# Kernel optimization log

Measured on AMD Instinct MI355X. Metric: run time of the kernel, lower is better.

Reference implementation:

```python
import jax, jax.numpy as jnp
import numpy as np

N_NODES = 100000
N_EDGES = 625000
D_IN = 128
D_OUT = 128


def setup_inputs() -> dict:
    key = jax.random.key(0)
    k1, k2, k3, k4, k5 = jax.random.split(key, 5)
    scale = 1.0 / np.sqrt(D_IN)
    x = jax.random.normal(k1, (N_NODES, D_IN), dtype=jnp.float32)
    edge_index = jax.random.randint(k2, (2, N_EDGES), 0, N_NODES, dtype=jnp.int64)
    W_l = jax.random.normal(k3, (D_IN, D_OUT), dtype=jnp.float32) * scale
    b_l = jax.random.normal(k4, (D_OUT,), dtype=jnp.float32) * scale
    W_r = jax.random.normal(k5, (D_IN, D_OUT), dtype=jnp.float32) * scale
    return {"x": x, "edge_index": edge_index, "W_l": W_l, "b_l": b_l, "W_r": W_r}


def reference(x, edge_index, W_l, b_l, W_r):
    # SAGEConv (mean aggr, no self loops):
    #   out = lin_l(mean_{j in N(i)} x_j) + lin_r(x_i)
    src = edge_index[0]  # message source nodes
    dst = edge_index[1]  # aggregation targets
    n = x.shape[0]
    msgs = x[src]  # [E, D_IN] gather
    agg = jax.ops.segment_sum(msgs, dst, num_segments=n)  # [N, D_IN]
    deg = jax.ops.segment_sum(jnp.ones_like(dst, dtype=x.dtype), dst, num_segments=n)
    mean = agg / jnp.maximum(deg, 1.0)[:, None]  # isolated nodes -> 0
    return mean @ W_l + b_l + x @ W_r
```

## Files before the change

### kernel.cpp

```cpp
#include <hip/hip_runtime.h>


constexpr int N_NODES = 100000;
constexpr int N_EDGES = 625000;
constexpr int D = 128;
constexpr int SCAN_CHUNK = 1024;
constexpr int N_SCAN_BLOCKS = (N_NODES + SCAN_CHUNK - 1) / SCAN_CHUNK;

typedef __attribute__((ext_vector_type(8))) short short8;
typedef __attribute__((ext_vector_type(4))) short short4v;
typedef __attribute__((ext_vector_type(4))) float f32x4;

__device__ __forceinline__ unsigned short f2bf(float f) {
    union { float f; unsigned int u; } c; c.f = f;
    unsigned int u = c.u + 0x7fffu + ((c.u >> 16) & 1u);
    return (unsigned short)(u >> 16);
}

__global__ __launch_bounds__(256) void csr_hist(
    const int* __restrict__ dst, int* __restrict__ cnt)
{
    int e = blockIdx.x * 256 + threadIdx.x;
    if (e < N_EDGES) atomicAdd(&cnt[dst[e]], 1);
}

__global__ __launch_bounds__(256) void scan_blocks(
    const int* __restrict__ cnt, int* __restrict__ ptr, int* __restrict__ bsums)
{
    __shared__ int sh[256];
    const int t = threadIdx.x;
    const int base = blockIdx.x * SCAN_CHUNK + t * 4;
    int v0 = (base + 0 < N_NODES) ? cnt[base + 0] : 0;
    int v1 = (base + 1 < N_NODES) ? cnt[base + 1] : 0;
    int v2 = (base + 2 < N_NODES) ? cnt[base + 2] : 0;
    int v3 = (base + 3 < N_NODES) ? cnt[base + 3] : 0;
    const int tsum = v0 + v1 + v2 + v3;
    sh[t] = tsum;
    __syncthreads();
    #pragma unroll
    for (int off = 1; off < 256; off <<= 1) {
        int val = (t >= off) ? sh[t - off] : 0;
        __syncthreads();
        sh[t] += val;
        __syncthreads();
    }
    const int texcl = sh[t] - tsum;
    if (t == 255) bsums[blockIdx.x] = sh[255];
    int e0 = texcl, e1 = e0 + v0, e2 = e1 + v1, e3 = e2 + v2;
    if (base + 0 < N_NODES) ptr[base + 0] = e0;
    if (base + 1 < N_NODES) ptr[base + 1] = e1;
    if (base + 2 < N_NODES) ptr[base + 2] = e2;
    if (base + 3 < N_NODES) ptr[base + 3] = e3;
}

__global__ __launch_bounds__(128) void scan_bsums(int* __restrict__ bsums)
{
    __shared__ int sh[128];
    const int t = threadIdx.x;
    int v = (t < N_SCAN_BLOCKS) ? bsums[t] : 0;
    sh[t] = v;
    __syncthreads();
    #pragma unroll
    for (int off = 1; off < 128; off <<= 1) {
        int val = (t >= off) ? sh[t - off] : 0;
        __syncthreads();
        sh[t] += val;
        __syncthreads();
    }
    if (t < N_SCAN_BLOCKS) bsums[t] = sh[t] - v;
}

__global__ __launch_bounds__(256) void add_offsets(
    int* __restrict__ ptr, int* __restrict__ cursor, const int* __restrict__ bsums)
{
    int i = blockIdx.x * 256 + threadIdx.x;
    if (i < N_NODES) {
        int p = ptr[i] + bsums[i >> 10];
        ptr[i] = p;
        cursor[i] = p;
    }
    if (i == 0) ptr[N_NODES] = N_EDGES;
}

__global__ __launch_bounds__(256) void csr_fill(
    const int* __restrict__ src, const int* __restrict__ dst,
    int* __restrict__ cursor, int* __restrict__ sorted_src)
{
    int e = blockIdx.x * 256 + threadIdx.x;
    if (e < N_EDGES) {
        int t = dst[e];
        int pos = atomicAdd(&cursor[t], 1);
        sorted_src[pos] = src[e];
    }
}

__global__ __launch_bounds__(256) void sage_aggregate(
    const float* __restrict__ x,
    const int* __restrict__ ptr,
    const int* __restrict__ sorted_src,
    float* __restrict__ mean)
{
    const int node = blockIdx.x * 4 + (threadIdx.x >> 6);
    if (node >= N_NODES) return;
    const int lane = threadIdx.x & 63;
    const int beg = ptr[node];
    const int end = ptr[node + 1];

    float2 acc0 = make_float2(0.f, 0.f);
    float2 acc1 = make_float2(0.f, 0.f);
    int i = beg;
    for (; i + 1 < end; i += 2) {
        int s0 = sorted_src[i];
        int s1 = sorted_src[i + 1];
        float2 a = *(const float2*)&x[(size_t)s0 * D + lane * 2];
        float2 b = *(const float2*)&x[(size_t)s1 * D + lane * 2];
        acc0.x += a.x; acc0.y += a.y;
        acc1.x += b.x; acc1.y += b.y;
    }
    if (i < end) {
        int s0 = sorted_src[i];
        float2 a = *(const float2*)&x[(size_t)s0 * D + lane * 2];
        acc0.x += a.x; acc0.y += a.y;
    }
    const float sc = 1.0f / fmaxf((float)(end - beg), 1.0f);
    float2 r = make_float2((acc0.x + acc1.x) * sc, (acc0.y + acc1.y) * sc);
    *(float2*)&mean[(size_t)node * D + lane * 2] = r;
}

__global__ __launch_bounds__(256) void wt_build(
    const float* __restrict__ Wl, const float* __restrict__ Wr,
    unsigned short* __restrict__ wT)
{
    int idx = blockIdx.x * 256 + threadIdx.x;
    if (idx >= 128 * 256) return;
    int n = idx >> 8;
    int k = idx & 255;
    float v = (k < 128) ? Wl[k * 128 + n] : Wr[(k - 128) * 128 + n];
    wT[n * 256 + k] = f2bf(v);
}

__global__ __launch_bounds__(256) void sage_gemm_mfma(
    const float* __restrict__ x,
    const unsigned short* __restrict__ wT,
    const float* __restrict__ bl,
    float* __restrict__ out)
{
    __shared__ unsigned short sW[128 * 256];
    __shared__ unsigned short sA[32 * 256];

    const int tid  = threadIdx.x;
    const int lane = tid & 63;
    const int w    = tid >> 6;
    const int l15  = lane & 15;
    const int lg   = lane >> 4;

    #pragma unroll
    for (int i = 0; i < 16; ++i) {
        int c  = tid + i * 256;
        int n  = c >> 5;
        int k8 = c & 31;
        short8 v = ((const short8*)wT)[c];
        *(short8*)&sW[n * 256 + ((k8 ^ (n & 7)) << 3)] = v;
    }

    const int a_r0 = l15;
    const int a_r1 = 16 + l15;
    const int n0 = w * 32 + l15;
    const int n1 = n0 + 16;
    const float bias0 = bl[n0];
    const float bias1 = bl[n1];

    const int nTiles = N_NODES / 32;

    for (int tile = blockIdx.x; tile < nTiles; tile += gridDim.x) {
        const int row0 = tile * 32;

        #pragma unroll
        for (int i = 0; i < 8; ++i) {
            int c    = tid + i * 256;
            int r    = c >> 6;
            int half = (c >> 5) & 1;
            int f4   = c & 31;
            const float* srcp = half ? &x[(size_t)(row0 + r) * D + f4 * 4]
                                     : &out[(size_t)(row0 + r) * D + f4 * 4];
            float4 v = *(const float4*)srcp;
            short4v b;
            b.x = (short)f2bf(v.x); b.y = (short)f2bf(v.y);
            b.z = (short)f2bf(v.z); b.w = (short)f2bf(v.w);
            int k = half * 128 + f4 * 4;
            int u = k >> 3;
            *(short4v*)&sA[r * 256 + ((u ^ (r & 7)) << 3) + (k & 7)] = b;
        }
        __syncthreads();

        f32x4 acc00 = {0.f,0.f,0.f,0.f}, acc01 = {0.f,0.f,0.f,0.f};
        f32x4 acc10 = {0.f,0.f,0.f,0.f}, acc11 = {0.f,0.f,0.f,0.f};

        #pragma unroll
        for (int s = 0; s < 8; ++s) {
            int ks = s * 4 + lg;
            short8 a0 = *(const short8*)&sA[a_r0 * 256 + ((ks ^ (a_r0 & 7)) << 3)];
            short8 a1 = *(const short8*)&sA[a_r1 * 256 + ((ks ^ (a_r1 & 7)) << 3)];
            short8 b0 = *(const short8*)&sW[n0 * 256 + ((ks ^ (n0 & 7)) << 3)];
            short8 b1 = *(const short8*)&sW[n1 * 256 + ((ks ^ (n1 & 7)) << 3)];
            acc00 = __builtin_amdgcn_mfma_f32_16x16x32_bf16(a0, b0, acc00, 0, 0, 0);
            acc01 = __builtin_amdgcn_mfma_f32_16x16x32_bf16(a0, b1, acc01, 0, 0, 0);
            acc10 = __builtin_amdgcn_mfma_f32_16x16x32_bf16(a1, b0, acc10, 0, 0, 0);
            acc11 = __builtin_amdgcn_mfma_f32_16x16x32_bf16(a1, b1, acc11, 0, 0, 0);
        }
        __syncthreads();

        #pragma unroll
        for (int reg = 0; reg < 4; ++reg) {
            int r0w = row0 + lg * 4 + reg;
            int r1w = r0w + 16;
            out[(size_t)r0w * D + n0] = acc00[reg] + bias0;
            out[(size_t)r0w * D + n1] = acc01[reg] + bias1;
            out[(size_t)r1w * D + n0] = acc10[reg] + bias0;
            out[(size_t)r1w * D + n1] = acc11[reg] + bias1;
        }
    }
}

__global__ __launch_bounds__(256) void sage_scatter(
    const float* __restrict__ x, const int* __restrict__ src,
    const int* __restrict__ dst, float* __restrict__ agg, float* __restrict__ deg)
{
    int gid = blockIdx.x * 256 + threadIdx.x;
    int e = gid >> 7;
    if (e >= N_EDGES) return;
    int d = gid & 127;
    atomicAdd(&agg[(size_t)dst[e] * D + d], x[(size_t)src[e] * D + d]);
    if (d == 0) atomicAdd(&deg[dst[e]], 1.0f);
}

__global__ __launch_bounds__(256) void apply_mean(
    float* __restrict__ agg, const float* __restrict__ deg)
{
    int gid = blockIdx.x * 256 + threadIdx.x;
    int row = gid >> 5;
    if (row >= N_NODES) return;
    float sc = 1.0f / fmaxf(deg[row], 1.0f);
    float4 v = ((float4*)agg)[gid];
    v.x *= sc; v.y *= sc; v.z *= sc; v.w *= sc;
    ((float4*)agg)[gid] = v;
}

__device__ __forceinline__ void accum_tile(
    float acc[4][4], const float (*sWf)[D], const float (*srow)[D], int h, int j4)
{
    #pragma unroll 2
    for (int k = 0; k < D; k += 4) {
        float4 w0 = *(const float4*)&sWf[k + 0][j4];
        float4 w1 = *(const float4*)&sWf[k + 1][j4];
        float4 w2 = *(const float4*)&sWf[k + 2][j4];
        float4 w3 = *(const float4*)&sWf[k + 3][j4];
        #pragma unroll
        for (int r = 0; r < 4; ++r) {
            float4 a = *(const float4*)&srow[h + r * 8][k];
            acc[r][0] = fmaf(a.x, w0.x, fmaf(a.y, w1.x, fmaf(a.z, w2.x, fmaf(a.w, w3.x, acc[r][0]))));
            acc[r][1] = fmaf(a.x, w0.y, fmaf(a.y, w1.y, fmaf(a.z, w2.y, fmaf(a.w, w3.y, acc[r][1]))));
            acc[r][2] = fmaf(a.x, w0.z, fmaf(a.y, w1.z, fmaf(a.z, w2.z, fmaf(a.w, w3.z, acc[r][2]))));
            acc[r][3] = fmaf(a.x, w0.w, fmaf(a.y, w1.w, fmaf(a.z, w2.w, fmaf(a.w, w3.w, acc[r][3]))));
        }
    }
}

__global__ __launch_bounds__(256) void sage_gemm_f32(
    const float* __restrict__ x, const float* __restrict__ Wl,
    const float* __restrict__ bl, const float* __restrict__ Wr,
    float* __restrict__ out)
{
    __shared__ float sWf[D][D];
    __shared__ float srow[32][D];
    const int tid = threadIdx.x;
    const int j4 = (tid & 31) * 4;
    const int h  = tid >> 5;
    const int nTiles = (N_NODES + 31) / 32;
    const float4 bias = *(const float4*)(bl + j4);

    for (int tile = blockIdx.x; tile < nTiles; tile += gridDim.x) {
        const int row0 = tile * 32;
        float acc[4][4];
        #pragma unroll
        for (int r = 0; r < 4; ++r)
            #pragma unroll
            for (int c = 0; c < 4; ++c) acc[r][c] = 0.0f;

        __syncthreads();
        #pragma unroll
        for (int i = 0; i < 16; ++i)
            ((float4*)sWf)[tid + i * 256] = ((const float4*)Wl)[tid + i * 256];
        #pragma unroll
        for (int i = 0; i < 4; ++i) {
            int idx = tid + i * 256, r = idx >> 5, c = idx & 31, row = row0 + r;
            float4 v = make_float4(0.f,0.f,0.f,0.f);
            if (row < N_NODES) v = ((const float4*)out)[(size_t)row * 32 + c];
            ((float4*)srow)[idx] = v;
        }
        __syncthreads();
        accum_tile(acc, sWf, srow, h, j4);

        __syncthreads();
        #pragma unroll
        for (int i = 0; i < 16; ++i)
            ((float4*)sWf)[tid + i * 256] = ((const float4*)Wr)[tid + i * 256];
        #pragma unroll
        for (int i = 0; i < 4; ++i) {
            int idx = tid + i * 256, r = idx >> 5, c = idx & 31, row = row0 + r;
            float4 v = make_float4(0.f,0.f,0.f,0.f);
            if (row < N_NODES) v = ((const float4*)x)[(size_t)row * 32 + c];
            ((float4*)srow)[idx] = v;
        }
        __syncthreads();
        accum_tile(acc, sWf, srow, h, j4);

        #pragma unroll
        for (int r = 0; r < 4; ++r) {
            int row = row0 + h + r * 8;
            if (row < N_NODES) {
                float4 v = make_float4(acc[r][0] + bias.x, acc[r][1] + bias.y,
                                       acc[r][2] + bias.z, acc[r][3] + bias.w);
                *(float4*)(out + (size_t)row * D + j4) = v;
            }
        }
    }
}

extern "C" void kernel_launch(void* const* d_in, const int* in_sizes, int n_in,
                              void* d_out, int out_size, void* d_ws, size_t ws_size,
                              hipStream_t stream) {
    const float* x   = (const float*)d_in[0];
    const int*   ei  = (const int*)d_in[1];
    const float* Wl  = (const float*)d_in[2];
    const float* bl  = (const float*)d_in[3];
    const float* Wr  = (const float*)d_in[4];
    float* out = (float*)d_out;

    const int* src = ei;
    const int* dst = ei + N_EDGES;

    int* cnt    = (int*)d_ws;
    int* ptr    = cnt + N_NODES;
    int* cursor = ptr + N_NODES + 1;
    int* bsums  = cursor + N_NODES;
    int* sorted = bsums + 128;
    size_t needed = (size_t)(3 * N_NODES + 1 + 128 + N_EDGES) * sizeof(int);

    if (ws_size >= needed) {
        hipMemsetAsync(cnt, 0, (size_t)N_NODES * sizeof(int), stream);
        csr_hist<<<(N_EDGES + 255) / 256, 256, 0, stream>>>(dst, cnt);
        scan_blocks<<<N_SCAN_BLOCKS, 256, 0, stream>>>(cnt, ptr, bsums);
        scan_bsums<<<1, 128, 0, stream>>>(bsums);
        add_offsets<<<(N_NODES + 255) / 256, 256, 0, stream>>>(ptr, cursor, bsums);
        csr_fill<<<(N_EDGES + 255) / 256, 256, 0, stream>>>(src, dst, cursor, sorted);

        unsigned short* wT = (unsigned short*)cursor;
        wt_build<<<(128 * 256 + 255) / 256, 256, 0, stream>>>(Wl, Wr, wT);

        sage_aggregate<<<(N_NODES + 3) / 4, 256, 0, stream>>>(x, ptr, sorted, out);
        sage_gemm_mfma<<<512, 256, 0, stream>>>(x, wT, bl, out);
    } else {
        float* deg = (float*)d_ws;
        hipMemsetAsync(out, 0, (size_t)N_NODES * D * sizeof(float), stream);
        hipMemsetAsync(deg, 0, (size_t)N_NODES * sizeof(float), stream);
        long long total = (long long)N_EDGES * 128;
        sage_scatter<<<(int)((total + 255) / 256), 256, 0, stream>>>(x, src, dst, out, deg);
        apply_mean<<<(N_NODES * 32 + 255) / 256, 256, 0, stream>>>(out, deg);
        sage_gemm_f32<<<512, 256, 0, stream>>>(x, Wl, bl, Wr, out);
    }
}
```

Measured before the change: 165.7 us.

## Convert x to bf16 once and gather/aggregate in bf16 with bf16 mean

Adds a pass that converts x to bf16 in the workspace. The neighbor-mean aggregation then gathers 4-byte bf16 pairs instead of 8-byte float pairs, unrolled by four, and writes the mean as bf16. The GEMM reads the bf16 mean and bf16 x directly into shared memory without per-tile conversion. The goal is to halve gather and GEMM input traffic. The cost is an extra conversion pass, a larger workspace (two bf16 N×D buffers) and slightly lower precision in the aggregated inputs.

Measured after the change: 154.2 us. 6.9% less time.

```diff
diff --git a/kernel.cpp b/kernel.cpp
--- a/kernel.cpp
+++ b/kernel.cpp
@@ -15,6 +15,12 @@
     union { float f; unsigned int u; } c; c.f = f;
     unsigned int u = c.u + 0x7fffu + ((c.u >> 16) & 1u);
     return (unsigned short)(u >> 16);
+}
+__device__ __forceinline__ float bflo(unsigned int v) {
+    union { unsigned int u; float f; } c; c.u = v << 16; return c.f;
+}
+__device__ __forceinline__ float bfhi(unsigned int v) {
+    union { unsigned int u; float f; } c; c.u = v & 0xffff0000u; return c.f;
 }
 
 __global__ __launch_bounds__(256) void csr_hist(
@@ -94,6 +100,183 @@
     }
 }
 
+__global__ __launch_bounds__(256) void x2bf(
+    const float* __restrict__ x, unsigned short* __restrict__ xb)
+{
+    int c = blockIdx.x * 256 + threadIdx.x;
+    if (c >= N_NODES * D / 8) return;
+    const float4* xp = (const float4*)x;
+    float4 a = xp[(size_t)c * 2];
+    float4 b = xp[(size_t)c * 2 + 1];
+    short8 v;
+    v[0] = (short)f2bf(a.x); v[1] = (short)f2bf(a.y);
+    v[2] = (short)f2bf(a.z); v[3] = (short)f2bf(a.w);
+    v[4] = (short)f2bf(b.x); v[5] = (short)f2bf(b.y);
+    v[6] = (short)f2bf(b.z); v[7] = (short)f2bf(b.w);
+    ((short8*)xb)[c] = v;
+}
+
+__global__ __launch_bounds__(256) void wt_build(
+    const float* __restrict__ Wl, const float* __restrict__ Wr,
+    unsigned short* __restrict__ wT)
+{
+    int idx = blockIdx.x * 256 + threadIdx.x;
+    if (idx >= 128 * 256) return;
+    int n = idx >> 8;
+    int k = idx & 255;
+    float v = (k < 128) ? Wl[k * 128 + n] : Wr[(k - 128) * 128 + n];
+    wT[n * 256 + k] = f2bf(v);
+}
+
+template<bool MBF>
+__global__ __launch_bounds__(256) void sage_aggregate_bf(
+    const unsigned short* __restrict__ xb,
+    const int* __restrict__ ptr,
+    const int* __restrict__ sorted_src,
+    unsigned short* __restrict__ mean_bf,
+    float* __restrict__ mean_f32)
+{
+    const int node = blockIdx.x * 4 + (threadIdx.x >> 6);
+    if (node >= N_NODES) return;
+    const int lane = threadIdx.x & 63;
+    const int beg = ptr[node];
+    const int end = ptr[node + 1];
+    const int off = lane * 2;
+
+    float a0 = 0.f, a1 = 0.f, b0 = 0.f, b1 = 0.f;
+    float c0 = 0.f, c1 = 0.f, d0 = 0.f, d1 = 0.f;
+    int i = beg;
+    for (; i + 3 < end; i += 4) {
+        int s0 = sorted_src[i], s1 = sorted_src[i + 1];
+        int s2 = sorted_src[i + 2], s3 = sorted_src[i + 3];
+        unsigned int v0 = *(const unsigned int*)&xb[(size_t)s0 * D + off];
+        unsigned int v1 = *(const unsigned int*)&xb[(size_t)s1 * D + off];
+        unsigned int v2 = *(const unsigned int*)&xb[(size_t)s2 * D + off];
+        unsigned int v3 = *(const unsigned int*)&xb[(size_t)s3 * D + off];
+        a0 += bflo(v0); a1 += bfhi(v0);
+        b0 += bflo(v1); b1 += bfhi(v1);
+        c0 += bflo(v2); c1 += bfhi(v2);
+        d0 += bflo(v3); d1 += bfhi(v3);
+    }
+    for (; i < end; ++i) {
+        int s0 = sorted_src[i];
+        unsigned int v0 = *(const unsigned int*)&xb[(size_t)s0 * D + off];
+        a0 += bflo(v0); a1 += bfhi(v0);
+    }
+    const float sc = 1.0f / fmaxf((float)(end - beg), 1.0f);
+    float r0 = ((a0 + b0) + (c0 + d0)) * sc;
+    float r1 = ((a1 + b1) + (c1 + d1)) * sc;
+    if (MBF) {
+        unsigned int r = (unsigned int)f2bf(r0) | ((unsigned int)f2bf(r1) << 16);
+        *(unsigned int*)&mean_bf[(size_t)node * D + off] = r;
+    } else {
+        *(float2*)&mean_f32[(size_t)node * D + off] = make_float2(r0, r1);
+    }
+}
+
+template<bool MBF>
+__global__ __launch_bounds__(256) void sage_gemm_bf(
+    const unsigned short* __restrict__ xb,
+    const unsigned short* __restrict__ mean_bf,
+    const unsigned short* __restrict__ wT,
+    const float* __restrict__ bl,
+    float* __restrict__ out)
+{
+    __shared__ unsigned short sW[128 * 256];
+    __shared__ unsigned short sA[32 * 256];
+
+    const int tid  = threadIdx.x;
+    const int lane = tid & 63;
+    const int w    = tid >> 6;
+    const int l15  = lane & 15;
+    const int lg   = lane >> 4;
+
+    #pragma unroll
+    for (int i = 0; i < 16; ++i) {
+        int c  = tid + i * 256;
+        int n  = c >> 5;
+        int k8 = c & 31;
+        short8 v = ((const short8*)wT)[c];
+        *(short8*)&sW[n * 256 + ((k8 ^ (n & 7)) << 3)] = v;
+    }
+
+    const int a_r0 = l15;
+    const int a_r1 = 16 + l15;
+    const int n0 = w * 32 + l15;
+    const int n1 = n0 + 16;
+    const float bias0 = bl[n0];
+    const float bias1 = bl[n1];
+
+    const int nTiles = N_NODES / 32;
+
+    for (int tile = blockIdx.x; tile < nTiles; tile += gridDim.x) {
+        const int row0 = tile * 32;
+
+        if constexpr (MBF) {
+            #pragma unroll
+            for (int i = 0; i < 4; ++i) {
+                int c = tid + i * 256;
+                int r = c >> 5;
+                int s = c & 31;
+                const unsigned short* srcp = (s < 16)
+                    ? &mean_bf[(size_t)(row0 + r) * D + s * 8]
+                    : &xb[(size_t)(row0 + r) * D + (s - 16) * 8];
+                short8 v = *(const short8*)srcp;
+                *(short8*)&sA[r * 256 + ((s ^ (r & 7)) << 3)] = v;
+            }
+        } else {
+            #pragma unroll
+            for (int i = 0; i < 4; ++i) {
+                int c = tid + i * 256;
+                int r = c >> 5;
+                int f4 = c & 31;
+                float4 v = *(const float4*)&out[(size_t)(row0 + r) * D + f4 * 4];
+                short4v b;
+                b.x = (short)f2bf(v.x); b.y = (short)f2bf(v.y);
+                b.z = (short)f2bf(v.z); b.w = (short)f2bf(v.w);
+                int u = f4 >> 1;
+                *(short4v*)&sA[r * 256 + ((u ^ (r & 7)) << 3) + (f4 & 1) * 4] = b;
+            }
+            #pragma unroll
+            for (int i = 0; i < 2; ++i) {
+                int c = tid + i * 256;
+                int r = c >> 4;
+                int s = 16 + (c & 15);
+                short8 v = *(const short8*)&xb[(size_t)(row0 + r) * D + (c & 15) * 8];
+                *(short8*)&sA[r * 256 + ((s ^ (r & 7)) << 3)] = v;
+            }
+        }
+        __syncthreads();
+
+        f32x4 acc00 = {0.f,0.f,0.f,0.f}, acc01 = {0.f,0.f,0.f,0.f};
+        f32x4 acc10 = {0.f,0.f,0.f,0.f}, acc11 = {0.f,0.f,0.f,0.f};
+
+        #pragma unroll
+        for (int s = 0; s < 8; ++s) {
+            int ks = s * 4 + lg;
+            short8 a0 = *(const short8*)&sA[a_r0 * 256 + ((ks ^ (a_r0 & 7)) << 3)];
+            short8 a1 = *(const short8*)&sA[a_r1 * 256 + ((ks ^ (a_r1 & 7)) << 3)];
+            short8 b0 = *(const short8*)&sW[n0 * 256 + ((ks ^ (n0 & 7)) << 3)];
+            short8 b1 = *(const short8*)&sW[n1 * 256 + ((ks ^ (n1 & 7)) << 3)];
+            acc00 = __builtin_amdgcn_mfma_f32_16x16x32_bf16(a0, b0, acc00, 0, 0, 0);
+            acc01 = __builtin_amdgcn_mfma_f32_16x16x32_bf16(a0, b1, acc01, 0, 0, 0);
+            acc10 = __builtin_amdgcn_mfma_f32_16x16x32_bf16(a1, b0, acc10, 0, 0, 0);
+            acc11 = __builtin_amdgcn_mfma_f32_16x16x32_bf16(a1, b1, acc11, 0, 0, 0);
+        }
+        __syncthreads();
+
+        #pragma unroll
+        for (int reg = 0; reg < 4; ++reg) {
+            int r0w = row0 + lg * 4 + reg;
+            int r1w = r0w + 16;
+            out[(size_t)r0w * D + n0] = acc00[reg] + bias0;
+            out[(size_t)r0w * D + n1] = acc01[reg] + bias1;
+            out[(size_t)r1w * D + n0] = acc10[reg] + bias0;
+            out[(size_t)r1w * D + n1] = acc11[reg] + bias1;
+        }
+    }
+}
+
 __global__ __launch_bounds__(256) void sage_aggregate(
     const float* __restrict__ x,
     const int* __restrict__ ptr,
@@ -127,18 +310,6 @@
     *(float2*)&mean[(size_t)node * D + lane * 2] = r;
 }
 
-__global__ __launch_bounds__(256) void wt_build(
-    const float* __restrict__ Wl, const float* __restrict__ Wr,
-    unsigned short* __restrict__ wT)
-{
-    int idx = blockIdx.x * 256 + threadIdx.x;
-    if (idx >= 128 * 256) return;
-    int n = idx >> 8;
-    int k = idx & 255;
-    float v = (k < 128) ? Wl[k * 128 + n] : Wr[(k - 128) * 128 + n];
-    wT[n * 256 + k] = f2bf(v);
-}
-
 __global__ __launch_bounds__(256) void sage_gemm_mfma(
     const float* __restrict__ x,
     const unsigned short* __restrict__ wT,
@@ -169,12 +340,10 @@
     const int n1 = n0 + 16;
     const float bias0 = bl[n0];
     const float bias1 = bl[n1];
-
     const int nTiles = N_NODES / 32;
 
     for (int tile = blockIdx.x; tile < nTiles; tile += gridDim.x) {
         const int row0 = tile * 32;
-
         #pragma unroll
         for (int i = 0; i < 8; ++i) {
             int c    = tid + i * 256;
@@ -345,9 +514,15 @@
     int* cursor = ptr + N_NODES + 1;
     int* bsums  = cursor + N_NODES;
     int* sorted = bsums + 128;
-    size_t needed = (size_t)(3 * N_NODES + 1 + 128 + N_EDGES) * sizeof(int);
-
-    if (ws_size >= needed) {
+    unsigned short* xb      = (unsigned short*)(sorted + N_EDGES);
+    unsigned short* mean_bf = xb + (size_t)N_NODES * D;
+
+    size_t base_ints = (size_t)(3 * N_NODES + 1 + 128 + N_EDGES);
+    size_t need_B  = base_ints * sizeof(int);
+    size_t need_A2 = need_B + (size_t)N_NODES * D * 2;
+    size_t need_A  = need_A2 + (size_t)N_NODES * D * 2;
+
+    if (ws_size >= need_B) {
         hipMemsetAsync(cnt, 0, (size_t)N_NODES * sizeof(int), stream);
         csr_hist<<<(N_EDGES + 255) / 256, 256, 0, stream>>>(dst, cnt);
         scan_blocks<<<N_SCAN_BLOCKS, 256, 0, stream>>>(cnt, ptr, bsums);
@@ -358,8 +533,20 @@
         unsigned short* wT = (unsigned short*)cursor;
         wt_build<<<(128 * 256 + 255) / 256, 256, 0, stream>>>(Wl, Wr, wT);
 
-        sage_aggregate<<<(N_NODES + 3) / 4, 256, 0, stream>>>(x, ptr, sorted, out);
-        sage_gemm_mfma<<<512, 256, 0, stream>>>(x, wT, bl, out);
+        if (ws_size >= need_A) {
+            x2bf<<<(N_NODES * D / 8 + 255) / 256, 256, 0, stream>>>(x, xb);
+            sage_aggregate_bf<true><<<(N_NODES + 3) / 4, 256, 0, stream>>>(
+                xb, ptr, sorted, mean_bf, nullptr);
+            sage_gemm_bf<true><<<512, 256, 0, stream>>>(xb, mean_bf, wT, bl, out);
+        } else if (ws_size >= need_A2) {
+            x2bf<<<(N_NODES * D / 8 + 255) / 256, 256, 0, stream>>>(x, xb);
+            sage_aggregate_bf<false><<<(N_NODES + 3) / 4, 256, 0, stream>>>(
+                xb, ptr, sorted, nullptr, out);
+            sage_gemm_bf<false><<<512, 256, 0, stream>>>(xb, nullptr, wT, bl, out);
+        } else {
+            sage_aggregate<<<(N_NODES + 3) / 4, 256, 0, stream>>>(x, ptr, sorted, out);
+            sage_gemm_mfma<<<512, 256, 0, stream>>>(x, wT, bl, out);
+        }
     } else {
         float* deg = (float*)d_ws;
         hipMemsetAsync(out, 0, (size_t)N_NODES * D * sizeof(float), stream);
```
